# Kernel optimization log

Measured on AMD Instinct MI355X. Metric: run time of the kernel, lower is better.

## Reference

```python
import jax, jax.numpy as jnp
import numpy as np

N = 50000   # num_nodes
E = 800000  # num_edges
IN, HID, OUT = 64, 96, 96
LN_EPS = 1e-5


def setup_inputs() -> dict:
    key = jax.random.key(0)
    ks = jax.random.split(key, 12)
    s = 0.05
    return {
        "x": jax.random.normal(ks[0], (N, IN), jnp.float32),
        "edge_index": jax.random.randint(ks[1], (2, E), 0, N, dtype=jnp.int64),
        "edge_weight": jax.random.uniform(ks[2], (E,), jnp.float32),
        "W0": jax.random.normal(ks[3], (IN, HID), jnp.float32) * s,
        "b0": jnp.zeros((HID,), jnp.float32),
        "ln_g": jnp.ones((HID,), jnp.float32),
        "ln_b": jnp.zeros((HID,), jnp.float32),
        "Ws": jax.random.normal(ks[4], (IN, HID), jnp.float32) * s,
        "bs": jnp.zeros((HID,), jnp.float32),
        "W1": jax.random.normal(ks[5], (HID, OUT), jnp.float32) * s,
        "b1": jnp.zeros((OUT,), jnp.float32),
    }


def _gcn(h, W, b, src, dst, ew, n):
    # GCNConv with add_self_loops=True and edge weights (PyG gcn_norm)
    loop = jnp.arange(n, dtype=src.dtype)
    s = jnp.concatenate([src, loop])
    d = jnp.concatenate([dst, loop])
    w = jnp.concatenate([ew, jnp.ones((n,), ew.dtype)])
    deg = jax.ops.segment_sum(w, d, num_segments=n)
    dinv = jnp.where(deg > 0, jax.lax.rsqrt(jnp.maximum(deg, 1e-12)), 0.0)
    norm = dinv[s] * w * dinv[d]                 # [E+N]
    msg = (h @ W)[s] * norm[:, None]             # gather transformed src feats
    return jax.ops.segment_sum(msg, d, num_segments=n) + b


def _layernorm(h, g, b):
    mu = h.mean(-1, keepdims=True)
    var = ((h - mu) ** 2).mean(-1, keepdims=True)
    return (h - mu) * jax.lax.rsqrt(var + LN_EPS) * g + b


def reference(x, edge_index, edge_weight, W0, b0, ln_g, ln_b, Ws, bs, W1, b1):
    src, dst = edge_index[0], edge_index[1]
    n = x.shape[0]
    # layer 0: GCN -> LayerNorm -> ReLU -> (dropout: eval no-op) -> +Linear skip
    h = _gcn(x, W0, b0, src, dst, edge_weight, n)
    h = jax.nn.relu(_layernorm(h, ln_g, ln_b))
    h = h + (x @ Ws + bs)
    # final layer: GCN only
    return _gcn(h, W1, b1, src, dst, edge_weight, n)
```

## Files before the change

### kernel.cpp

```cpp
#include <hip/hip_runtime.h>

#define LN_EPS 1e-5f

__device__ __forceinline__ float bflo(unsigned u) { union { unsigned u; float f; } c; c.u = u << 16; return c.f; }
__device__ __forceinline__ float bfhi(unsigned u) { union { unsigned u; float f; } c; c.u = u & 0xffff0000u; return c.f; }
__device__ __forceinline__ unsigned f2bfbits(float f) {
    union { float f; unsigned u; } c; c.f = f;
    return (c.u + 0x7fffu + ((c.u >> 16) & 1u)) >> 16;
}
__device__ __forceinline__ unsigned packbf(float lo, float hi) {
    return f2bfbits(lo) | (f2bfbits(hi) << 16);
}

__global__ void init_kernel(int* __restrict__ cnt, int n) {
    int i = blockIdx.x * 256 + threadIdx.x;
    if (i < n) cnt[i] = 0;
}

__global__ void cnt_rank_kernel(const int* __restrict__ dst, int* __restrict__ cnt,
                                int* __restrict__ rank, int e) {
    int i = blockIdx.x * 256 + threadIdx.x;
    if (i >= e) return;
    rank[i] = atomicAdd(&cnt[dst[i]], 1);
}

__global__ void cvtprep_kernel(const float* __restrict__ x, unsigned* __restrict__ xb2, int total4,
                               const float* __restrict__ W0, const float* __restrict__ Ws,
                               const float* __restrict__ W1,
                               float4* __restrict__ w0i, float4* __restrict__ wsi,
                               float4* __restrict__ w1i, int gX) {
    if ((int)blockIdx.x < gX) {
        int i = blockIdx.x * 256 + threadIdx.x;
        if (i >= total4) return;
        float4 v = ((const float4*)x)[i];
        uint2 o;
        o.x = packbf(v.x, v.y);
        o.y = packbf(v.z, v.w);
        ((uint2*)xb2)[i] = o;
    } else {
        int i = (blockIdx.x - gX) * 256 + threadIdx.x;
        if (i < 1536) {
            int kq = i / 96, j = i % 96;
            const float* p = W0 + kq * 4 * 96 + j;
            w0i[i] = make_float4(p[0], p[96], p[192], p[288]);
            const float* q = Ws + kq * 4 * 96 + j;
            wsi[i] = make_float4(q[0], q[96], q[192], q[288]);
        }
        int i2 = i - 1536;
        if (i2 >= 0 && i2 < 2304) {
            int kq = i2 / 96, j = i2 % 96;
            const float* p = W1 + kq * 4 * 96 + j;
            w1i[i2] = make_float4(p[0], p[96], p[192], p[288]);
        }
    }
}

__global__ void blocksum_kernel(const int* __restrict__ cnt, int* __restrict__ bsum, int n) {
    int base = blockIdx.x * 1024;
    int t = threadIdx.x;
    int i0 = base + t * 4;
    int s = 0;
    if (i0 + 3 < n) { int4 v = *(const int4*)(cnt + i0); s = v.x + v.y + v.z + v.w; }
    else { for (int k = 0; k < 4; ++k) if (i0 + k < n) s += cnt[i0 + k]; }
    #pragma unroll
    for (int off = 32; off; off >>= 1) s += __shfl_xor(s, off);
    __shared__ int wsum[4];
    if ((t & 63) == 0) wsum[t >> 6] = s;
    __syncthreads();
    if (t == 0) bsum[blockIdx.x] = wsum[0] + wsum[1] + wsum[2] + wsum[3];
}

__global__ void scan_bsum_kernel(const int* __restrict__ bsum, int* __restrict__ boff, int nb) {
    int t = threadIdx.x;
    int carry = 0;
    for (int base = 0; base < nb; base += 64) {
        int i = base + t;
        int v = (i < nb) ? bsum[i] : 0;
        int sc = v;
        #pragma unroll
        for (int off = 1; off < 64; off <<= 1) {
            int u = __shfl_up(sc, off);
            if (t >= off) sc += u;
        }
        if (i < nb) boff[i] = carry + sc - v;
        carry += __shfl(sc, 63);
    }
}

__global__ void rowptr_kernel(const int* __restrict__ cnt, const int* __restrict__ boff,
                              int* __restrict__ rowptr, int n, int etot) {
    __shared__ int wsum[4];
    int b = blockIdx.x;
    int t = threadIdx.x;
    int i0 = b * 1024 + t * 4;
    int c0 = 0, c1 = 0, c2 = 0, c3 = 0;
    if (i0 < n)     c0 = cnt[i0];
    if (i0 + 1 < n) c1 = cnt[i0 + 1];
    if (i0 + 2 < n) c2 = cnt[i0 + 2];
    if (i0 + 3 < n) c3 = cnt[i0 + 3];
    int tot = c0 + c1 + c2 + c3;
    int lane = t & 63, w = t >> 6;
    int sc = tot;
    #pragma unroll
    for (int off = 1; off < 64; off <<= 1) {
        int u = __shfl_up(sc, off);
        if (lane >= off) sc += u;
    }
    if (lane == 63) wsum[w] = sc;
    __syncthreads();
    int woff = 0;
    for (int k = 0; k < w; ++k) woff += wsum[k];
    int excl = boff[b] + woff + sc - tot;
    if (i0 < n)     rowptr[i0]     = excl;
    if (i0 + 1 < n) rowptr[i0 + 1] = excl + c0;
    if (i0 + 2 < n) rowptr[i0 + 2] = excl + c0 + c1;
    if (i0 + 3 < n) rowptr[i0 + 3] = excl + c0 + c1 + c2;
    if (b == 0 && t == 0) rowptr[n] = etot;
}

__global__ void scatter_part_kernel(const int* __restrict__ src, const int* __restrict__ dst,
                                    const float* __restrict__ ew, const int* __restrict__ rank,
                                    const int* __restrict__ rowptr,
                                    uint2* __restrict__ cv, int e, int n) {
    int part = blockIdx.x & 7;
    int blk  = blockIdx.x >> 3;
    int chunk = (n + 7) >> 3;
    int lo = part * chunk;
    int hi = lo + chunk; if (hi > n) hi = n;
    int stride = (gridDim.x >> 3) * 256;
    for (int i = blk * 256 + threadIdx.x; i < e; i += stride) {
        int d = dst[i];
        if (d >= lo && d < hi) {
            int pos = rowptr[d] + rank[i];
            cv[pos] = make_uint2((unsigned)src[i], __float_as_uint(ew[i]));
        }
    }
}

__global__ void degsum_kernel(const int* __restrict__ rowptr, const uint2* __restrict__ cv,
                              float* __restrict__ dinv, int n) {
    int i = blockIdx.x * 256 + threadIdx.x;
    if (i >= n) return;
    int p0 = rowptr[i], p1 = rowptr[i + 1];
    float s = 1.0f;
    for (int p = p0; p < p1; ++p) s += __uint_as_float(cv[p].y);
    dinv[i] = rsqrtf(s);
}

__global__ void agg64_kernel(const unsigned* __restrict__ xb, const float* __restrict__ dinv,
                             const int* __restrict__ rowptr, const uint2* __restrict__ cv,
                             float* __restrict__ aggX, int n) {
    int node = blockIdx.x * 4 + (threadIdx.x >> 6);
    if (node >= n) return;
    int lane = threadIdx.x & 63;
    int g = lane >> 4, l4 = lane & 15;
    const uint2* x2 = (const uint2*)xb;
    int p0 = rowptr[node], pe = rowptr[node + 1];
    float a0 = 0, a1 = 0, a2 = 0, a3 = 0;
    float b0 = 0, b1 = 0, b2 = 0, b3 = 0;
    for (int p = p0 + g; p < pe; p += 8) {
        uint2 e1 = cv[p];
        int s1 = (int)e1.x;
        float w1 = __uint_as_float(e1.y) * dinv[s1];
        uint2 r1 = x2[(size_t)s1 * 16 + l4];
        bool h2 = (p + 4) < pe;
        uint2 e2 = h2 ? cv[p + 4] : e1;
        int s2 = (int)e2.x;
        float w2 = h2 ? __uint_as_float(e2.y) * dinv[s2] : 0.0f;
        uint2 r2 = x2[(size_t)s2 * 16 + l4];
        a0 = fmaf(w1, bflo(r1.x), a0); a1 = fmaf(w1, bfhi(r1.x), a1);
        a2 = fmaf(w1, bflo(r1.y), a2); a3 = fmaf(w1, bfhi(r1.y), a3);
        b0 = fmaf(w2, bflo(r2.x), b0); b1 = fmaf(w2, bfhi(r2.x), b1);
        b2 = fmaf(w2, bflo(r2.y), b2); b3 = fmaf(w2, bfhi(r2.y), b3);
    }
    a0 += b0; a1 += b1; a2 += b2; a3 += b3;
    #pragma unroll
    for (int off = 16; off <= 32; off <<= 1) {
        a0 += __shfl_xor(a0, off);
        a1 += __shfl_xor(a1, off);
        a2 += __shfl_xor(a2, off);
        a3 += __shfl_xor(a3, off);
    }
    if (g == 0) {
        float di = dinv[node];
        uint2 sr = x2[(size_t)node * 16 + l4];
        a0 = fmaf(di, bflo(sr.x), a0); a1 = fmaf(di, bfhi(sr.x), a1);
        a2 = fmaf(di, bflo(sr.y), a2); a3 = fmaf(di, bfhi(sr.y), a3);
        ((float4*)(aggX + (size_t)node * 64))[l4] =
            make_float4(a0 * di, a1 * di, a2 * di, a3 * di);
    }
}

__global__ __launch_bounds__(512) void gemm_ln_kernel(
        const float4* __restrict__ w0i, const float4* __restrict__ wsi,
        const float* __restrict__ aggX, const float* __restrict__ x,
        const float* __restrict__ b0,
        const float* __restrict__ ln_g, const float* __restrict__ ln_b,
        const float* __restrict__ bs,
        unsigned short* __restrict__ hb, int n) {
    __shared__ float4 w0s[1536];
    __shared__ float4 wss[1536];
    __shared__ float4 ar[1024];
    __shared__ float4 xr[1024];
    int t = threadIdx.x;
    int base = blockIdx.x * 64;
    for (int i = t; i < 1536; i += 512) { w0s[i] = w0i[i]; wss[i] = wsi[i]; }
    int rem = n - base; if (rem > 64) rem = 64;
    int nf4 = rem * 16;
    for (int i = t; i < nf4; i += 512) {
        ar[i] = ((const float4*)(aggX + (size_t)base * 64))[i];
        xr[i] = ((const float4*)(x + (size_t)base * 64))[i];
    }
    __syncthreads();
    int hw = t >> 5;
    int l = t & 31;
    int r0 = hw * 4;
    float acc[4][3] = {{0.f,0.f,0.f},{0.f,0.f,0.f},{0.f,0.f,0.f},{0.f,0.f,0.f}};
    float sk[4][3]  = {{0.f,0.f,0.f},{0.f,0.f,0.f},{0.f,0.f,0.f},{0.f,0.f,0.f}};
    for (int kq = 0; kq < 16; ++kq) {
        float4 wa = w0s[kq * 96 + l];
        float4 wb = w0s[kq * 96 + l + 32];
        float4 wc = w0s[kq * 96 + l + 64];
        float4 sa = wss[kq * 96 + l];
        float4 sb = wss[kq * 96 + l + 32];
        float4 scv = wss[kq * 96 + l + 64];
        #pragma unroll
        for (int r = 0; r < 4; ++r) {
            float4 a  = ar[(r0 + r) * 16 + kq];
            float4 xv = xr[(r0 + r) * 16 + kq];
            acc[r][0] = fmaf(a.w, wa.w, fmaf(a.z, wa.z, fmaf(a.y, wa.y, fmaf(a.x, wa.x, acc[r][0]))));
            acc[r][1] = fmaf(a.w, wb.w, fmaf(a.z, wb.z, fmaf(a.y, wb.y, fmaf(a.x, wb.x, acc[r][1]))));
            acc[r][2] = fmaf(a.w, wc.w, fmaf(a.z, wc.z, fmaf(a.y, wc.y, fmaf(a.x, wc.x, acc[r][2]))));
            sk[r][0]  = fmaf(xv.w, sa.w, fmaf(xv.z, sa.z, fmaf(xv.y, sa.y, fmaf(xv.x, sa.x, sk[r][0]))));
            sk[r][1]  = fmaf(xv.w, sb.w, fmaf(xv.z, sb.z, fmaf(xv.y, sb.y, fmaf(xv.x, sb.x, sk[r][1]))));
            sk[r][2]  = fmaf(xv.w, scv.w, fmaf(xv.z, scv.z, fmaf(xv.y, scv.y, fmaf(xv.x, scv.x, sk[r][2]))));
        }
    }
    float b00 = b0[l], b01 = b0[l + 32], b02 = b0[l + 64];
    float g0 = ln_g[l], g1 = ln_g[l + 32], g2 = ln_g[l + 64];
    float e0 = ln_b[l], e1 = ln_b[l + 32], e2 = ln_b[l + 64];
    float q0 = bs[l],   q1 = bs[l + 32],   q2 = bs[l + 64];
    #pragma unroll
    for (int r = 0; r < 4; ++r) {
        int node = base + r0 + r;
        if (node >= n) break;
        float a0v = acc[r][0] + b00, a1v = acc[r][1] + b01, a2v = acc[r][2] + b02;
        float s1 = a0v + a1v + a2v;
        #pragma unroll
        for (int off = 1; off < 32; off <<= 1) s1 += __shfl_xor(s1, off);
        float mu = s1 * (1.0f / 96.0f);
        float d0 = a0v - mu, d1 = a1v - mu, d2 = a2v - mu;
        float sq = d0 * d0 + d1 * d1 + d2 * d2;
        #pragma unroll
        for (int off = 1; off < 32; off <<= 1) sq += __shfl_xor(sq, off);
        float rinv = rsqrtf(sq * (1.0f / 96.0f) + LN_EPS);
        float v0 = fmaxf(d0 * rinv * g0 + e0, 0.0f) + sk[r][0] + q0;
        float v1 = fmaxf(d1 * rinv * g1 + e1, 0.0f) + sk[r][1] + q1;
        float v2 = fmaxf(d2 * rinv * g2 + e2, 0.0f) + sk[r][2] + q2;
        unsigned short* o = hb + (size_t)node * 96;
        o[l]      = (unsigned short)f2bfbits(v0);
        o[l + 32] = (unsigned short)f2bfbits(v1);
        o[l + 64] = (unsigned short)f2bfbits(v2);
    }
}

__global__ void agg96_kernel(const unsigned short* __restrict__ hb, const float* __restrict__ dinv,
                             const int* __restrict__ rowptr, const uint2* __restrict__ cv,
                             float* __restrict__ aggH, int n) {
    int node = blockIdx.x * 4 + (threadIdx.x >> 6);
    if (node >= n) return;
    int lane = threadIdx.x & 63;
    int g = lane >> 4, l4 = lane & 15;
    const uint4* h4 = (const uint4*)hb;
    int p0 = rowptr[node], pe = rowptr[node + 1];
    float a0=0,a1=0,a2=0,a3=0,a4=0,a5=0,a6=0,a7=0;
    if (l4 < 12) {
        float c0=0,c1=0,c2=0,c3=0,c4=0,c5=0,c6=0,c7=0;
        for (int p = p0 + g; p < pe; p += 8) {
            uint2 e1 = cv[p];
            int s1 = (int)e1.x;
            float w1 = __uint_as_float(e1.y) * dinv[s1];
            uint4 r1 = h4[(size_t)s1 * 12 + l4];
            bool h2 = (p + 4) < pe;
            uint2 e2 = h2 ? cv[p + 4] : e1;
            int s2 = (int)e2.x;
            float w2 = h2 ? __uint_as_float(e2.y) * dinv[s2] : 0.0f;
            uint4 r2 = h4[(size_t)s2 * 12 + l4];
            a0 = fmaf(w1, bflo(r1.x), a0); a1 = fmaf(w1, bfhi(r1.x), a1);
            a2 = fmaf(w1, bflo(r1.y), a2); a3 = fmaf(w1, bfhi(r1.y), a3);
            a4 = fmaf(w1, bflo(r1.z), a4); a5 = fmaf(w1, bfhi(r1.z), a5);
            a6 = fmaf(w1, bflo(r1.w), a6); a7 = fmaf(w1, bfhi(r1.w), a7);
            c0 = fmaf(w2, bflo(r2.x), c0); c1 = fmaf(w2, bfhi(r2.x), c1);
            c2 = fmaf(w2, bflo(r2.y), c2); c3 = fmaf(w2, bfhi(r2.y), c3);
            c4 = fmaf(w2, bflo(r2.z), c4); c5 = fmaf(w2, bfhi(r2.z), c5);
            c6 = fmaf(w2, bflo(r2.w), c6); c7 = fmaf(w2, bfhi(r2.w), c7);
        }
        a0+=c0; a1+=c1; a2+=c2; a3+=c3; a4+=c4; a5+=c5; a6+=c6; a7+=c7;
    }
    #pragma unroll
    for (int off = 16; off <= 32; off <<= 1) {
        a0 += __shfl_xor(a0, off); a1 += __shfl_xor(a1, off);
        a2 += __shfl_xor(a2, off); a3 += __shfl_xor(a3, off);
        a4 += __shfl_xor(a4, off); a5 += __shfl_xor(a5, off);
        a6 += __shfl_xor(a6, off); a7 += __shfl_xor(a7, off);
    }
    if (g == 0 && l4 < 12) {
        float di = dinv[node];
        uint4 sr = h4[(size_t)node * 12 + l4];
        a0 = fmaf(di, bflo(sr.x), a0); a1 = fmaf(di, bfhi(sr.x), a1);
        a2 = fmaf(di, bflo(sr.y), a2); a3 = fmaf(di, bfhi(sr.y), a3);
        a4 = fmaf(di, bflo(sr.z), a4); a5 = fmaf(di, bfhi(sr.z), a5);
        a6 = fmaf(di, bflo(sr.w), a6); a7 = fmaf(di, bfhi(sr.w), a7);
        float4* o = (float4*)(aggH + (size_t)node * 96);
        o[l4 * 2]     = make_float4(a0 * di, a1 * di, a2 * di, a3 * di);
        o[l4 * 2 + 1] = make_float4(a4 * di, a5 * di, a6 * di, a7 * di);
    }
}

__global__ __launch_bounds__(512) void gemm_out_kernel(
        const float4* __restrict__ w1i, const float* __restrict__ aggH,
        const float* __restrict__ b1, float* __restrict__ out, int n) {
    __shared__ float4 w1s[2304];
    __shared__ float4 hr[1536];
    int t = threadIdx.x;
    int base = blockIdx.x * 64;
    for (int i = t; i < 2304; i += 512) w1s[i] = w1i[i];
    int rem = n - base; if (rem > 64) rem = 64;
    int nf4 = rem * 24;
    for (int i = t; i < nf4; i += 512)
        hr[i] = ((const float4*)(aggH + (size_t)base * 96))[i];
    __syncthreads();
    int hw = t >> 5, l = t & 31;
    int r0 = hw * 4;
    float acc[4][3] = {{0.f,0.f,0.f},{0.f,0.f,0.f},{0.f,0.f,0.f},{0.f,0.f,0.f}};
    for (int kq = 0; kq < 24; ++kq) {
        float4 wa = w1s[kq * 96 + l];
        float4 wb = w1s[kq * 96 + l + 32];
        float4 wc = w1s[kq * 96 + l + 64];
        #pragma unroll
        for (int r = 0; r < 4; ++r) {
            float4 a = hr[(r0 + r) * 24 + kq];
            acc[r][0] = fmaf(a.w, wa.w, fmaf(a.z, wa.z, fmaf(a.y, wa.y, fmaf(a.x, wa.x, acc[r][0]))));
            acc[r][1] = fmaf(a.w, wb.w, fmaf(a.z, wb.z, fmaf(a.y, wb.y, fmaf(a.x, wb.x, acc[r][1]))));
            acc[r][2] = fmaf(a.w, wc.w, fmaf(a.z, wc.z, fmaf(a.y, wc.y, fmaf(a.x, wc.x, acc[r][2]))));
        }
    }
    float c0 = b1[l], c1 = b1[l + 32], c2 = b1[l + 64];
    #pragma unroll
    for (int r = 0; r < 4; ++r) {
        int node = base + r0 + r;
        if (node >= n) break;
        float* o = out + (size_t)node * 96;
        o[l]      = acc[r][0] + c0;
        o[l + 32] = acc[r][1] + c1;
        o[l + 64] = acc[r][2] + c2;
    }
}

extern "C" void kernel_launch(void* const* d_in, const int* in_sizes, int n_in,
                              void* d_out, int out_size, void* d_ws, size_t ws_size,
                              hipStream_t stream) {
    const float* x    = (const float*)d_in[0];
    const int*   ei   = (const int*)d_in[1];
    const float* ew   = (const float*)d_in[2];
    const float* W0   = (const float*)d_in[3];
    const float* b0   = (const float*)d_in[4];
    const float* ln_g = (const float*)d_in[5];
    const float* ln_b = (const float*)d_in[6];
    const float* Ws   = (const float*)d_in[7];
    const float* bs   = (const float*)d_in[8];
    const float* W1   = (const float*)d_in[9];
    const float* b1   = (const float*)d_in[10];
    float* out = (float*)d_out;

    const int E = in_sizes[2];
    const int N = in_sizes[0] / 64;
    const int* src = ei;
    const int* dst = ei + E;

    char* ws = (char*)d_ws;
    size_t off = 0;
    auto alloc = [&](size_t bytes) -> void* {
        void* p = ws + off;
        off = (off + bytes + 255) & ~(size_t)255;
        return p;
    };
    float* dinv   = (float*)alloc((size_t)N * 4);
    int*   cnt    = (int*)alloc((size_t)N * 4);
    int*   rowptr = (int*)alloc((size_t)(N + 1) * 4);
    int*   rank   = (int*)alloc((size_t)E * 4);
    int*   bsum   = (int*)alloc((size_t)256 * 4);
    int*   boff   = (int*)alloc((size_t)256 * 4);
    uint2* cv     = (uint2*)alloc((size_t)E * 8);
    unsigned* xb  = (unsigned*)alloc((size_t)N * 64 * 2);
    unsigned short* hb = (unsigned short*)alloc((size_t)N * 96 * 2);
    float* bufA   = (float*)alloc((size_t)N * 96 * 4);
    float4* w0i   = (float4*)alloc((size_t)1536 * 16);
    float4* wsi   = (float4*)alloc((size_t)1536 * 16);
    float4* w1i   = (float4*)alloc((size_t)2304 * 16);

    int gN = (N + 255) / 256;
    int gE = (E + 255) / 256;
    int nb = (N + 1023) / 1024;
    int gX = (N * 16 + 255) / 256;
    int gP = 8 * 128;

    init_kernel<<<gN, 256, 0, stream>>>(cnt, N);
    cnt_rank_kernel<<<gE, 256, 0, stream>>>(dst, cnt, rank, E);
    cvtprep_kernel<<<gX + 15, 256, 0, stream>>>(x, xb, N * 16, W0, Ws, W1, w0i, wsi, w1i, gX);
    blocksum_kernel<<<nb, 256, 0, stream>>>(cnt, bsum, N);
    scan_bsum_kernel<<<1, 64, 0, stream>>>(bsum, boff, nb);
    rowptr_kernel<<<nb, 256, 0, stream>>>(cnt, boff, rowptr, N, E);
    scatter_part_kernel<<<gP, 256, 0, stream>>>(src, dst, ew, rank, rowptr, cv, E, N);
    degsum_kernel<<<gN, 256, 0, stream>>>(rowptr, cv, dinv, N);

    int gA = (N + 3) / 4;
    agg64_kernel<<<gA, 256, 0, stream>>>(xb, dinv, rowptr, cv, bufA, N);

    int gG = (N + 63) / 64;
    gemm_ln_kernel<<<gG, 512, 0, stream>>>(w0i, wsi, bufA, x, b0, ln_g, ln_b, bs, hb, N);

    agg96_kernel<<<gA, 256, 0, stream>>>(hb, dinv, rowptr, cv, bufA, N);

    gemm_out_kernel<<<gG, 512, 0, stream>>>(w1i, bufA, b1, out, N);
}
```

Measured before the change: 218.4 us.

## Fuse second aggregation with output GEMM and fold count init into prep

Merges the layer-1 neighbour aggregation and the final W1 projection into one kernel. Each wavefront aggregates one node into shared memory and then multiplies it by W1 held in LDS, so the fp32 intermediate no longer goes to global memory and back. It also moves the zeroing of the count buffer into the existing convert/prep launch, removing one launch. In exchange, every 16-node block reloads the whole W1 tile into LDS, and the 1024-thread blocks with about 42KB of LDS may limit occupancy.

```diff
diff --git a/kernel.cpp b/kernel.cpp
--- a/kernel.cpp
+++ b/kernel.cpp
@@ -12,11 +12,6 @@
     return f2bfbits(lo) | (f2bfbits(hi) << 16);
 }
 
-__global__ void init_kernel(int* __restrict__ cnt, int n) {
-    int i = blockIdx.x * 256 + threadIdx.x;
-    if (i < n) cnt[i] = 0;
-}
-
 __global__ void cnt_rank_kernel(const int* __restrict__ dst, int* __restrict__ cnt,
                                 int* __restrict__ rank, int e) {
     int i = blockIdx.x * 256 + threadIdx.x;
@@ -28,17 +23,19 @@
                                const float* __restrict__ W0, const float* __restrict__ Ws,
                                const float* __restrict__ W1,
                                float4* __restrict__ w0i, float4* __restrict__ wsi,
-                               float4* __restrict__ w1i, int gX) {
-    if ((int)blockIdx.x < gX) {
-        int i = blockIdx.x * 256 + threadIdx.x;
+                               float4* __restrict__ w1i, int* __restrict__ cnt,
+                               int n, int gX) {
+    int b = (int)blockIdx.x;
+    if (b < gX) {
+        int i = b * 256 + threadIdx.x;
         if (i >= total4) return;
         float4 v = ((const float4*)x)[i];
         uint2 o;
         o.x = packbf(v.x, v.y);
         o.y = packbf(v.z, v.w);
         ((uint2*)xb2)[i] = o;
-    } else {
-        int i = (blockIdx.x - gX) * 256 + threadIdx.x;
+    } else if (b < gX + 15) {
+        int i = (b - gX) * 256 + threadIdx.x;
         if (i < 1536) {
             int kq = i / 96, j = i % 96;
             const float* p = W0 + kq * 4 * 96 + j;
@@ -52,6 +49,10 @@
             const float* p = W1 + kq * 4 * 96 + j;
             w1i[i2] = make_float4(p[0], p[96], p[192], p[288]);
         }
+    } else {
+        int i4 = ((b - gX - 15) * 256 + threadIdx.x) * 4;
+        if (i4 + 3 < n) *(int4*)(cnt + i4) = make_int4(0, 0, 0, 0);
+        else for (int k = i4; k < n; ++k) cnt[k] = 0;
     }
 }
 
@@ -264,18 +265,26 @@
     }
 }
 
-__global__ void agg96_kernel(const unsigned short* __restrict__ hb, const float* __restrict__ dinv,
-                             const int* __restrict__ rowptr, const uint2* __restrict__ cv,
-                             float* __restrict__ aggH, int n) {
-    int node = blockIdx.x * 4 + (threadIdx.x >> 6);
+__global__ __launch_bounds__(1024) void agg96_out_kernel(
+        const unsigned short* __restrict__ hb, const float* __restrict__ dinv,
+        const int* __restrict__ rowptr, const uint2* __restrict__ cv,
+        const float4* __restrict__ w1i, const float* __restrict__ b1,
+        float* __restrict__ out, int n) {
+    __shared__ float4 w1s[2304];
+    __shared__ float4 hr[384];
+    int t = threadIdx.x;
+    for (int i = t; i < 2304; i += 1024) w1s[i] = w1i[i];
+    __syncthreads();
+    int w = t >> 6;
+    int node = blockIdx.x * 16 + w;
     if (node >= n) return;
-    int lane = threadIdx.x & 63;
+    int lane = t & 63;
     int g = lane >> 4, l4 = lane & 15;
     const uint4* h4 = (const uint4*)hb;
     int p0 = rowptr[node], pe = rowptr[node + 1];
     float a0=0,a1=0,a2=0,a3=0,a4=0,a5=0,a6=0,a7=0;
+    float c0=0,c1=0,c2=0,c3=0,c4=0,c5=0,c6=0,c7=0;
     if (l4 < 12) {
-        float c0=0,c1=0,c2=0,c3=0,c4=0,c5=0,c6=0,c7=0;
         for (int p = p0 + g; p < pe; p += 8) {
             uint2 e1 = cv[p];
             int s1 = (int)e1.x;
@@ -311,50 +320,23 @@
         a2 = fmaf(di, bflo(sr.y), a2); a3 = fmaf(di, bfhi(sr.y), a3);
         a4 = fmaf(di, bflo(sr.z), a4); a5 = fmaf(di, bfhi(sr.z), a5);
         a6 = fmaf(di, bflo(sr.w), a6); a7 = fmaf(di, bfhi(sr.w), a7);
-        float4* o = (float4*)(aggH + (size_t)node * 96);
-        o[l4 * 2]     = make_float4(a0 * di, a1 * di, a2 * di, a3 * di);
-        o[l4 * 2 + 1] = make_float4(a4 * di, a5 * di, a6 * di, a7 * di);
-    }
-}
-
-__global__ __launch_bounds__(512) void gemm_out_kernel(
-        const float4* __restrict__ w1i, const float* __restrict__ aggH,
-        const float* __restrict__ b1, float* __restrict__ out, int n) {
-    __shared__ float4 w1s[2304];
-    __shared__ float4 hr[1536];
-    int t = threadIdx.x;
-    int base = blockIdx.x * 64;
-    for (int i = t; i < 2304; i += 512) w1s[i] = w1i[i];
-    int rem = n - base; if (rem > 64) rem = 64;
-    int nf4 = rem * 24;
-    for (int i = t; i < nf4; i += 512)
-        hr[i] = ((const float4*)(aggH + (size_t)base * 96))[i];
-    __syncthreads();
-    int hw = t >> 5, l = t & 31;
-    int r0 = hw * 4;
-    float acc[4][3] = {{0.f,0.f,0.f},{0.f,0.f,0.f},{0.f,0.f,0.f},{0.f,0.f,0.f}};
+        hr[w * 24 + l4 * 2]     = make_float4(a0 * di, a1 * di, a2 * di, a3 * di);
+        hr[w * 24 + l4 * 2 + 1] = make_float4(a4 * di, a5 * di, a6 * di, a7 * di);
+    }
+    __threadfence_block();
+    int j2 = 64 + (lane & 31);
+    float accA = 0.f, accB = 0.f;
+    #pragma unroll 4
     for (int kq = 0; kq < 24; ++kq) {
-        float4 wa = w1s[kq * 96 + l];
-        float4 wb = w1s[kq * 96 + l + 32];
-        float4 wc = w1s[kq * 96 + l + 64];
-        #pragma unroll
-        for (int r = 0; r < 4; ++r) {
-            float4 a = hr[(r0 + r) * 24 + kq];
-            acc[r][0] = fmaf(a.w, wa.w, fmaf(a.z, wa.z, fmaf(a.y, wa.y, fmaf(a.x, wa.x, acc[r][0]))));
-            acc[r][1] = fmaf(a.w, wb.w, fmaf(a.z, wb.z, fmaf(a.y, wb.y, fmaf(a.x, wb.x, acc[r][1]))));
-            acc[r][2] = fmaf(a.w, wc.w, fmaf(a.z, wc.z, fmaf(a.y, wc.y, fmaf(a.x, wc.x, acc[r][2]))));
-        }
-    }
-    float c0 = b1[l], c1 = b1[l + 32], c2 = b1[l + 64];
-    #pragma unroll
-    for (int r = 0; r < 4; ++r) {
-        int node = base + r0 + r;
-        if (node >= n) break;
-        float* o = out + (size_t)node * 96;
-        o[l]      = acc[r][0] + c0;
-        o[l + 32] = acc[r][1] + c1;
-        o[l + 64] = acc[r][2] + c2;
-    }
+        float4 a  = hr[w * 24 + kq];
+        float4 wa = w1s[kq * 96 + lane];
+        float4 wb = w1s[kq * 96 + j2];
+        accA = fmaf(a.w, wa.w, fmaf(a.z, wa.z, fmaf(a.y, wa.y, fmaf(a.x, wa.x, accA))));
+        accB = fmaf(a.w, wb.w, fmaf(a.z, wb.z, fmaf(a.y, wb.y, fmaf(a.x, wb.x, accB))));
+    }
+    float* o = out + (size_t)node * 96;
+    o[lane] = accA + b1[lane];
+    if (lane < 32) o[j2] = accB + b1[j2];
 }
 
 extern "C" void kernel_launch(void* const* d_in, const int* in_sizes, int n_in,
@@ -403,11 +385,12 @@
     int gE = (E + 255) / 256;
     int nb = (N + 1023) / 1024;
     int gX = (N * 16 + 255) / 256;
+    int gC = (N / 4 + 255) / 256;
     int gP = 8 * 128;
 
-    init_kernel<<<gN, 256, 0, stream>>>(cnt, N);
+    cvtprep_kernel<<<gX + 15 + gC, 256, 0, stream>>>(x, xb, N * 16, W0, Ws, W1,
+                                                     w0i, wsi, w1i, cnt, N, gX);
     cnt_rank_kernel<<<gE, 256, 0, stream>>>(dst, cnt, rank, E);
-    cvtprep_kernel<<<gX + 15, 256, 0, stream>>>(x, xb, N * 16, W0, Ws, W1, w0i, wsi, w1i, gX);
     blocksum_kernel<<<nb, 256, 0, stream>>>(cnt, bsum, N);
     scan_bsum_kernel<<<1, 64, 0, stream>>>(bsum, boff, nb);
     rowptr_kernel<<<nb, 256, 0, stream>>>(cnt, boff, rowptr, N, E);
@@ -420,7 +403,6 @@
     int gG = (N + 63) / 64;
     gemm_ln_kernel<<<gG, 512, 0, stream>>>(w0i, wsi, bufA, x, b0, ln_g, ln_b, bs, hb, N);
 
-    agg96_kernel<<<gA, 256, 0, stream>>>(hb, dinv, rowptr, cv, bufA, N);
-
-    gemm_out_kernel<<<gG, 512, 0, stream>>>(w1i, bufA, b1, out, N);
-}
+    int gF = (N + 15) / 16;
+    agg96_out_kernel<<<gF, 1024, 0, stream>>>(hb, dinv, rowptr, cv, w1i, b1, out, N);
+}
```

New measurement: 210.5 us. -3.6%, faster.
